# Performance work log

Measured on AMD Instinct MI355X. Metric: run time of the kernel, lower is better.

## Reference

```python
import jax, jax.numpy as jnp
import numpy as np
import math

N_HEADS = 16
D_Q = 1024
D_K = 1024
D_V = 1024
D_OUT = 1024
HID = D_OUT // N_HEADS  # 64
BATCH = 2
SEQ = 2048


def setup_inputs() -> dict:
    key = jax.random.key(0)
    ks = jax.random.split(key, 7)
    stdv = 1.0 / math.sqrt(HID)
    so = 1.0 / math.sqrt(D_OUT)
    return {
        "q": jax.random.normal(ks[0], (BATCH, SEQ, D_Q), dtype=jnp.float32),
        "k": jax.random.normal(ks[1], (BATCH, SEQ, D_K), dtype=jnp.float32),
        "v": jax.random.normal(ks[2], (BATCH, SEQ, D_V), dtype=jnp.float32),
        "W_query": jax.random.uniform(ks[3], (N_HEADS, D_Q, HID), jnp.float32, -stdv, stdv),
        "W_key": jax.random.uniform(ks[4], (N_HEADS, D_K, HID), jnp.float32, -stdv, stdv),
        "W_val": jax.random.uniform(ks[5], (N_HEADS, D_V, HID), jnp.float32, -stdv, stdv),
        "W_out": jax.random.uniform(ks[6], (N_HEADS, HID, D_OUT), jnp.float32, -so, so),
    }


def reference(q, k, v, W_query, W_key, W_val, W_out):
    norm = 1.0 / math.sqrt(HID)
    # per-head projections: [h, b, s, e]
    Q = jnp.einsum("bqd,hde->hbqe", q, W_query)
    K = jnp.einsum("bkd,hde->hbke", k, W_key)
    V = jnp.einsum("bkd,hde->hbke", v, W_val)
    # scaled dot-product attention
    compat = norm * jnp.einsum("hbqe,hbke->hbqk", Q, K)
    attn = jax.nn.softmax(compat, axis=-1)
    heads = jnp.einsum("hbqk,hbke->hbqe", attn, V)
    # output projection: concat heads then W_out == sum over h of per-head proj
    out = jnp.einsum("hbqe,heo->bqo", heads, W_out)
    return out
```

## Files before the change

### kernel.cpp

```cpp
#include <hip/hip_runtime.h>
#include <hip/hip_bf16.h>

typedef __bf16 bf16;
typedef __bf16 bf16x8 __attribute__((ext_vector_type(8)));
typedef __bf16 bf16x4 __attribute__((ext_vector_type(4)));
typedef float  f32x4  __attribute__((ext_vector_type(4)));

#define MFMA16(a,b,c) __builtin_amdgcn_mfma_f32_16x16x32_bf16(a, b, c, 0, 0, 0)

__device__ __forceinline__ void gl2lds16(const bf16* g, bf16* l) {
    __builtin_amdgcn_global_load_lds(
        (__attribute__((address_space(1))) void*)g,
        (__attribute__((address_space(3))) void*)l, 16, 0, 0);
}

__global__ __launch_bounds__(256)
void prep_kernel(const float* __restrict__ q, const float* __restrict__ k,
                 const float* __restrict__ v, const float* __restrict__ Wq,
                 const float* __restrict__ Wk, const float* __restrict__ Wv,
                 const float* __restrict__ Wo, bf16* __restrict__ Xcat,
                 bf16* __restrict__ Wqkv, bf16* __restrict__ Wot)
{
    __shared__ bf16 Tl[64][72];
    const int bid = blockIdx.x;
    const int tid = threadIdx.x;

    if (bid < 6144) {
        int gidx = bid * 256 + tid;
        int t    = gidx >> 19;
        int off  = (gidx & 0x7FFFF) * 8;
        const float* src = (t == 0) ? q : (t == 1) ? k : v;
        const float4 f0 = *(const float4*)&src[off];
        const float4 f1 = *(const float4*)&src[off + 4];
        bf16x8 p = { (bf16)f0.x, (bf16)f0.y, (bf16)f0.z, (bf16)f0.w,
                     (bf16)f1.x, (bf16)f1.y, (bf16)f1.z, (bf16)f1.w };
        *(bf16x8*)&Xcat[(size_t)gidx * 8] = p;
        return;
    }
    if (bid < 6912) {
        int idx = bid - 6144;
        int x = idx & 15, z = idx >> 4;
        int t = z >> 4, h = z & 15;
        const float* inp = ((t == 0) ? Wq : (t == 1) ? Wk : Wv) + (size_t)h * 65536;
        bf16* outp = Wqkv + (size_t)t * 1024 * 1024 + (size_t)h * 65536;
        int r0 = x * 64;
        #pragma unroll
        for (int i = 0; i < 2; i++) {
            int s = tid + i * 256;
            int r = s >> 3, c8 = (s & 7) * 8;
            const float* ap = &inp[(size_t)(r0 + r) * 64 + c8];
            float4 f0 = *(const float4*)ap;
            float4 f1 = *(const float4*)(ap + 4);
            bf16x8 p = { (bf16)f0.x, (bf16)f0.y, (bf16)f0.z, (bf16)f0.w,
                         (bf16)f1.x, (bf16)f1.y, (bf16)f1.z, (bf16)f1.w };
            *(bf16x8*)&Tl[r][c8] = p;
        }
        __syncthreads();
        #pragma unroll
        for (int i = 0; i < 2; i++) {
            int s = tid + i * 256;
            int c = s >> 3, r8 = (s & 7) * 8;
            bf16x8 p;
            #pragma unroll
            for (int j = 0; j < 8; j++) p[j] = Tl[r8 + j][c];
            *(bf16x8*)&outp[(size_t)c * 1024 + r0 + r8] = p;
        }
        return;
    }
    {
        int idx = bid - 6912;
        int y = idx & 15, h = idx >> 4;
        int c0 = y * 64;
        const float* inp = Wo + (size_t)h * 65536;
        bf16* outp = Wot + (size_t)h * 64;
        #pragma unroll
        for (int i = 0; i < 2; i++) {
            int s = tid + i * 256;
            int r = s >> 3, c8 = (s & 7) * 8;
            const float* ap = &inp[(size_t)r * 1024 + c0 + c8];
            float4 f0 = *(const float4*)ap;
            float4 f1 = *(const float4*)(ap + 4);
            bf16x8 p = { (bf16)f0.x, (bf16)f0.y, (bf16)f0.z, (bf16)f0.w,
                         (bf16)f1.x, (bf16)f1.y, (bf16)f1.z, (bf16)f1.w };
            *(bf16x8*)&Tl[r][c8] = p;
        }
        __syncthreads();
        #pragma unroll
        for (int i = 0; i < 2; i++) {
            int s = tid + i * 256;
            int c = s >> 3, r8 = (s & 7) * 8;
            bf16x8 p;
            #pragma unroll
            for (int j = 0; j < 8; j++) p[j] = Tl[r8 + j][c];
            *(bf16x8*)&outp[(size_t)(c0 + c) * 1024 + r8] = p;
        }
    }
}

__global__ __launch_bounds__(256)
void qkv_gemm(const bf16* __restrict__ Xcat, const bf16* __restrict__ Wqkv,
              bf16* __restrict__ Cq, bf16* __restrict__ Ck, bf16* __restrict__ Vt,
              float qscale)
{
    __shared__ bf16 Al[128 * 64];
    __shared__ bf16 Bl[128 * 64];
    const int slab  = blockIdx.x >> 5;
    const int mbase = (blockIdx.x & 31) * 128;
    const int nbase = blockIdx.y * 128;
    const int tid = threadIdx.x;
    const int w = tid >> 6, lane = tid & 63;
    const int lm = lane & 15, q4 = lane >> 4;
    const int wr = (w >> 1) * 64, wc = (w & 1) * 64;
    const int lrow = lane >> 3, lsw = ((lane & 7) ^ lrow) * 8;

    const bf16* A  = Xcat + (size_t)slab * 4096 * 1024;
    const bf16* Bt = Wqkv + (size_t)slab * 1024 * 1024;

    f32x4 acc[4][4] = {};

    for (int k0 = 0; k0 < 1024; k0 += 64) {
        __syncthreads();
        #pragma unroll
        for (int i = 0; i < 4; i++) {
            int c = w * 4 + i;
            gl2lds16(&A [(size_t)(mbase + c * 8 + lrow) * 1024 + k0 + lsw], &Al[c * 512]);
            gl2lds16(&Bt[(size_t)(nbase + c * 8 + lrow) * 1024 + k0 + lsw], &Bl[c * 512]);
        }
        __syncthreads();
        #pragma unroll
        for (int kk2 = 0; kk2 < 2; kk2++) {
            bf16x8 a[4], bfr[4];
            const int g = ((kk2 * 4 + q4) ^ (lm & 7)) * 8;
            #pragma unroll
            for (int i = 0; i < 4; i++) a[i]   = *(const bf16x8*)&Al[(wr + i * 16 + lm) * 64 + g];
            #pragma unroll
            for (int j = 0; j < 4; j++) bfr[j] = *(const bf16x8*)&Bl[(wc + j * 16 + lm) * 64 + g];
            #pragma unroll
            for (int i = 0; i < 4; i++)
                #pragma unroll
                for (int j = 0; j < 4; j++)
                    acc[i][j] = MFMA16(a[i], bfr[j], acc[i][j]);
        }
    }

    if (slab == 2) {
        #pragma unroll
        for (int i = 0; i < 4; i++)
            #pragma unroll
            for (int j = 0; j < 4; j++) {
                int s0  = mbase + wr + i * 16 + q4 * 4;
                int col = nbase + wc + j * 16 + lm;
                int sp  = (s0 & ~31) | (((s0 >> 2) & 3) * 8) | (((s0 >> 4) & 1) * 4);
                bf16x4 p = { (bf16)acc[i][j][0], (bf16)acc[i][j][1],
                             (bf16)acc[i][j][2], (bf16)acc[i][j][3] };
                *(bf16x4*)&Vt[(size_t)col * 4096 + sp] = p;
            }
    } else {
        bf16* C = (slab == 0) ? Cq : Ck;
        const float scale = (slab == 0) ? qscale : 1.0f;
        #pragma unroll
        for (int i = 0; i < 4; i++)
            #pragma unroll
            for (int j = 0; j < 4; j++)
                #pragma unroll
                for (int r = 0; r < 4; r++) {
                    int row = mbase + wr + i * 16 + q4 * 4 + r;
                    int col = nbase + wc + j * 16 + lm;
                    C[(size_t)row * 1024 + col] = (bf16)(acc[i][j][r] * scale);
                }
    }
}

__global__ __launch_bounds__(256)
void outproj_gemm(const bf16* __restrict__ A, const bf16* __restrict__ Bt,
                  float* __restrict__ C)
{
    __shared__ bf16 Al[64 * 64];
    __shared__ bf16 Bl[128 * 64];
    const int mbase = blockIdx.x * 64;
    const int nbase = blockIdx.y * 128;
    const int tid = threadIdx.x;
    const int w = tid >> 6, lane = tid & 63;
    const int lm = lane & 15, q4 = lane >> 4;
    const int wm = (w >> 1) * 32, wn = (w & 1) * 64;
    const int lrow = lane >> 3, lsw = ((lane & 7) ^ lrow) * 8;

    f32x4 acc[2][4] = {};

    for (int k0 = 0; k0 < 1024; k0 += 64) {
        __syncthreads();
        #pragma unroll
        for (int i = 0; i < 2; i++) {
            int c = w * 2 + i;
            gl2lds16(&A[(size_t)(mbase + c * 8 + lrow) * 1024 + k0 + lsw], &Al[c * 512]);
        }
        #pragma unroll
        for (int i = 0; i < 4; i++) {
            int c = w * 4 + i;
            gl2lds16(&Bt[(size_t)(nbase + c * 8 + lrow) * 1024 + k0 + lsw], &Bl[c * 512]);
        }
        __syncthreads();
        #pragma unroll
        for (int kk2 = 0; kk2 < 2; kk2++) {
            bf16x8 a[2], bfr[4];
            const int g = ((kk2 * 4 + q4) ^ (lm & 7)) * 8;
            #pragma unroll
            for (int i = 0; i < 2; i++) a[i]   = *(const bf16x8*)&Al[(wm + i * 16 + lm) * 64 + g];
            #pragma unroll
            for (int j = 0; j < 4; j++) bfr[j] = *(const bf16x8*)&Bl[(wn + j * 16 + lm) * 64 + g];
            #pragma unroll
            for (int i = 0; i < 2; i++)
                #pragma unroll
                for (int j = 0; j < 4; j++)
                    acc[i][j] = MFMA16(a[i], bfr[j], acc[i][j]);
        }
    }

    #pragma unroll
    for (int i = 0; i < 2; i++)
        #pragma unroll
        for (int j = 0; j < 4; j++)
            #pragma unroll
            for (int r = 0; r < 4; r++) {
                int row = mbase + wm + i * 16 + q4 * 4 + r;
                int col = nbase + wn + j * 16 + lm;
                C[(size_t)row * 1024 + col] = acc[i][j][r];
            }
}

__global__ __launch_bounds__(256, 4)
void attn_kernel(const bf16* __restrict__ Qp, const bf16* __restrict__ Kp,
                 const bf16* __restrict__ Vt, bf16* __restrict__ Hd)
{
    __shared__ bf16 Kl[2][64 * 64];
    __shared__ bf16 Vl[2][64 * 64];

    const int n  = blockIdx.x + 32 * (blockIdx.y + 2 * blockIdx.z);
    const int m  = (n & 7) * 128 + (n >> 3);
    const int qt = m & 31, bh = m >> 5;
    const int b  = bh & 1,  h  = bh >> 1;

    const int qbase = qt * 64;
    const int tid  = threadIdx.x;
    const int w    = tid >> 6, lane = tid & 63;
    const int p    = w & 1;
    const int kvh  = w >> 1;
    const int lm   = lane & 15, q4 = lane >> 4;
    const int lrow = lane >> 3, lsw = ((lane & 7) ^ lrow) * 8;

    const bf16* Qh = Qp + (size_t)(b * 2048 + qbase + p * 32) * 1024 + h * 64;
    const bf16* Kh = Kp + (size_t)(b * 2048) * 1024 + h * 64;
    const bf16* Vh = Vt + (size_t)(h * 64) * 4096 + b * 2048;

    bf16x8 Qf[2][2];
    #pragma unroll
    for (int i = 0; i < 2; i++)
        #pragma unroll
        for (int kk2 = 0; kk2 < 2; kk2++)
            Qf[i][kk2] = *(const bf16x8*)&Qh[(size_t)(i * 16 + lm) * 1024 + kk2 * 32 + q4 * 8];

    const bf16 one = (bf16)1.0f;
    const bf16x8 ones = { one, one, one, one, one, one, one, one };

    f32x4 O[2][4] = {};
    f32x4 Lacc[2] = {};

    auto stage = [&](int kt, int d) {
        #pragma unroll
        for (int i = 0; i < 2; i++) {
            int c = w * 2 + i;
            gl2lds16(&Kh[(size_t)(kt * 64 + c * 8 + lrow) * 1024 + lsw], &Kl[d][c * 512]);
            gl2lds16(&Vh[(size_t)(c * 8 + lrow) * 4096 + kt * 64 + lsw], &Vl[d][c * 512]);
        }
    };

    stage(0, 0);

    for (int it = 0; it < 32; it++) {
        __syncthreads();
        if (it < 31) stage(it + 1, (it + 1) & 1);
        const bf16* Kd = &Kl[it & 1][0];
        const bf16* Vd = &Vl[it & 1][0];

        f32x4 St[2][2] = {};
        __builtin_amdgcn_s_setprio(1);
        #pragma unroll
        for (int c2 = 0; c2 < 2; c2++) {
            const int ctp = kvh * 2 + c2;
            #pragma unroll
            for (int kk2 = 0; kk2 < 2; kk2++) {
                const int g = ((kk2 * 4 + q4) ^ (lm & 7)) * 8;
                bf16x8 kf = *(const bf16x8*)&Kd[(ctp * 16 + lm) * 64 + g];
                #pragma unroll
                for (int i = 0; i < 2; i++)
                    St[i][c2] = MFMA16(kf, Qf[i][kk2], St[i][c2]);
            }
        }
        __builtin_amdgcn_s_setprio(0);

        bf16x8 Pf[2];
        #pragma unroll
        for (int i = 0; i < 2; i++)
            #pragma unroll
            for (int j = 0; j < 8; j++)
                Pf[i][j] = (bf16)__builtin_amdgcn_exp2f(St[i][j >> 2][j & 3]);

        __builtin_amdgcn_s_setprio(1);
        #pragma unroll
        for (int i = 0; i < 2; i++) Lacc[i] = MFMA16(Pf[i], ones, Lacc[i]);
        const int gv = ((kvh * 4 + q4) ^ (lm & 7)) * 8;
        #pragma unroll
        for (int et = 0; et < 4; et++) {
            bf16x8 vf = *(const bf16x8*)&Vd[(et * 16 + lm) * 64 + gv];
            #pragma unroll
            for (int i = 0; i < 2; i++)
                O[i][et] = MFMA16(Pf[i], vf, O[i][et]);
        }
        __builtin_amdgcn_s_setprio(0);
    }

    __syncthreads();
    float* Ol = (float*)&Kl[0][0];
    float* Ll = (float*)&Vl[0][0];
    if (kvh == 1) {
        #pragma unroll
        for (int i = 0; i < 2; i++)
            #pragma unroll
            for (int et = 0; et < 4; et++)
                #pragma unroll
                for (int r = 0; r < 4; r++)
                    Ol[p * 2048 + (i * 16 + q4 * 4 + r) * 64 + et * 16 + lm] = O[i][et][r];
        if (lm == 0) {
            #pragma unroll
            for (int i = 0; i < 2; i++)
                #pragma unroll
                for (int r = 0; r < 4; r++)
                    Ll[p * 32 + i * 16 + q4 * 4 + r] = Lacc[i][r];
        }
    }
    __syncthreads();
    if (kvh == 0) {
        #pragma unroll
        for (int i = 0; i < 2; i++) {
            float rl[4];
            #pragma unroll
            for (int r = 0; r < 4; r++)
                rl[r] = 1.0f / (Lacc[i][r] + Ll[p * 32 + i * 16 + q4 * 4 + r]);
            #pragma unroll
            for (int et = 0; et < 4; et++)
                #pragma unroll
                for (int r = 0; r < 4; r++) {
                    float o = O[i][et][r] +
                              Ol[p * 2048 + (i * 16 + q4 * 4 + r) * 64 + et * 16 + lm];
                    int row = b * 2048 + qbase + p * 32 + i * 16 + q4 * 4 + r;
                    Hd[(size_t)row * 1024 + h * 64 + et * 16 + lm] = (bf16)(o * rl[r]);
                }
        }
    }
}

extern "C" void kernel_launch(void* const* d_in, const int* in_sizes, int n_in,
                              void* d_out, int out_size, void* d_ws, size_t ws_size,
                              hipStream_t stream)
{
    const float* q  = (const float*)d_in[0];
    const float* k  = (const float*)d_in[1];
    const float* v  = (const float*)d_in[2];
    const float* Wq = (const float*)d_in[3];
    const float* Wk = (const float*)d_in[4];
    const float* Wv = (const float*)d_in[5];
    const float* Wo = (const float*)d_in[6];
    float* out = (float*)d_out;

    const size_t Mi = 1024 * 1024;
    bf16* Xcat  = (bf16*)d_ws;
    bf16* Hd    = Xcat;
    bf16* Wqkv  = Xcat + 12 * Mi;
    bf16* Wot   = Xcat + 15 * Mi;
    bf16* Qproj = Xcat + 16 * Mi;
    bf16* Kproj = Xcat + 20 * Mi;
    bf16* Vtb   = (bf16*)d_out;

    const float qscale = 0.125f * 1.4426950408889634f;

    prep_kernel<<<7168, 256, 0, stream>>>(q, k, v, Wq, Wk, Wv, Wo, Xcat, Wqkv, Wot);
    qkv_gemm<<<dim3(96, 8), 256, 0, stream>>>(Xcat, Wqkv, Qproj, Kproj, Vtb, qscale);
    attn_kernel<<<dim3(32, 2, 16), 256, 0, stream>>>(Qproj, Kproj, Vtb, Hd);
    outproj_gemm<<<dim3(64, 8), 256, 0, stream>>>(Hd, Wot, out);
}
```

Before: 211.0 us.

## Double-buffer LDS tiles in QKV and output-projection GEMMs

Both projection GEMMs now keep two LDS buffers per operand. The global-to-LDS load for the next k-tile is issued right after the barrier, so it overlaps with the MFMA work on the current tile, and there is one barrier per iteration instead of two. Wave priority is raised around the MFMA section. The cost is double the shared memory: 64KB per block in the QKV GEMM, which may lower occupancy.

```diff
diff --git a/kernel.cpp b/kernel.cpp
--- a/kernel.cpp
+++ b/kernel.cpp
@@ -102,8 +102,8 @@
               bf16* __restrict__ Cq, bf16* __restrict__ Ck, bf16* __restrict__ Vt,
               float qscale)
 {
-    __shared__ bf16 Al[128 * 64];
-    __shared__ bf16 Bl[128 * 64];
+    __shared__ bf16 Al[2][128 * 64];
+    __shared__ bf16 Bl[2][128 * 64];
     const int slab  = blockIdx.x >> 5;
     const int mbase = (blockIdx.x & 31) * 128;
     const int nbase = blockIdx.y * 128;
@@ -118,29 +118,38 @@
 
     f32x4 acc[4][4] = {};
 
-    for (int k0 = 0; k0 < 1024; k0 += 64) {
-        __syncthreads();
+    auto stage = [&](int k0, int d) {
         #pragma unroll
         for (int i = 0; i < 4; i++) {
             int c = w * 4 + i;
-            gl2lds16(&A [(size_t)(mbase + c * 8 + lrow) * 1024 + k0 + lsw], &Al[c * 512]);
-            gl2lds16(&Bt[(size_t)(nbase + c * 8 + lrow) * 1024 + k0 + lsw], &Bl[c * 512]);
-        }
+            gl2lds16(&A [(size_t)(mbase + c * 8 + lrow) * 1024 + k0 + lsw], &Al[d][c * 512]);
+            gl2lds16(&Bt[(size_t)(nbase + c * 8 + lrow) * 1024 + k0 + lsw], &Bl[d][c * 512]);
+        }
+    };
+
+    stage(0, 0);
+
+    for (int t = 0; t < 16; t++) {
         __syncthreads();
+        if (t < 15) stage((t + 1) * 64, (t + 1) & 1);
+        const bf16* Ad = &Al[t & 1][0];
+        const bf16* Bd = &Bl[t & 1][0];
+        __builtin_amdgcn_s_setprio(1);
         #pragma unroll
         for (int kk2 = 0; kk2 < 2; kk2++) {
             bf16x8 a[4], bfr[4];
             const int g = ((kk2 * 4 + q4) ^ (lm & 7)) * 8;
             #pragma unroll
-            for (int i = 0; i < 4; i++) a[i]   = *(const bf16x8*)&Al[(wr + i * 16 + lm) * 64 + g];
-            #pragma unroll
-            for (int j = 0; j < 4; j++) bfr[j] = *(const bf16x8*)&Bl[(wc + j * 16 + lm) * 64 + g];
+            for (int i = 0; i < 4; i++) a[i]   = *(const bf16x8*)&Ad[(wr + i * 16 + lm) * 64 + g];
+            #pragma unroll
+            for (int j = 0; j < 4; j++) bfr[j] = *(const bf16x8*)&Bd[(wc + j * 16 + lm) * 64 + g];
             #pragma unroll
             for (int i = 0; i < 4; i++)
                 #pragma unroll
                 for (int j = 0; j < 4; j++)
                     acc[i][j] = MFMA16(a[i], bfr[j], acc[i][j]);
         }
+        __builtin_amdgcn_s_setprio(0);
     }
 
     if (slab == 2) {
@@ -175,8 +184,8 @@
 void outproj_gemm(const bf16* __restrict__ A, const bf16* __restrict__ Bt,
                   float* __restrict__ C)
 {
-    __shared__ bf16 Al[64 * 64];
-    __shared__ bf16 Bl[128 * 64];
+    __shared__ bf16 Al[2][64 * 64];
+    __shared__ bf16 Bl[2][128 * 64];
     const int mbase = blockIdx.x * 64;
     const int nbase = blockIdx.y * 128;
     const int tid = threadIdx.x;
@@ -187,33 +196,42 @@
 
     f32x4 acc[2][4] = {};
 
-    for (int k0 = 0; k0 < 1024; k0 += 64) {
-        __syncthreads();
+    auto stage = [&](int k0, int d) {
         #pragma unroll
         for (int i = 0; i < 2; i++) {
             int c = w * 2 + i;
-            gl2lds16(&A[(size_t)(mbase + c * 8 + lrow) * 1024 + k0 + lsw], &Al[c * 512]);
+            gl2lds16(&A[(size_t)(mbase + c * 8 + lrow) * 1024 + k0 + lsw], &Al[d][c * 512]);
         }
         #pragma unroll
         for (int i = 0; i < 4; i++) {
             int c = w * 4 + i;
-            gl2lds16(&Bt[(size_t)(nbase + c * 8 + lrow) * 1024 + k0 + lsw], &Bl[c * 512]);
-        }
+            gl2lds16(&Bt[(size_t)(nbase + c * 8 + lrow) * 1024 + k0 + lsw], &Bl[d][c * 512]);
+        }
+    };
+
+    stage(0, 0);
+
+    for (int t = 0; t < 16; t++) {
         __syncthreads();
+        if (t < 15) stage((t + 1) * 64, (t + 1) & 1);
+        const bf16* Ad = &Al[t & 1][0];
+        const bf16* Bd = &Bl[t & 1][0];
+        __builtin_amdgcn_s_setprio(1);
         #pragma unroll
         for (int kk2 = 0; kk2 < 2; kk2++) {
             bf16x8 a[2], bfr[4];
             const int g = ((kk2 * 4 + q4) ^ (lm & 7)) * 8;
             #pragma unroll
-            for (int i = 0; i < 2; i++) a[i]   = *(const bf16x8*)&Al[(wm + i * 16 + lm) * 64 + g];
-            #pragma unroll
-            for (int j = 0; j < 4; j++) bfr[j] = *(const bf16x8*)&Bl[(wn + j * 16 + lm) * 64 + g];
+            for (int i = 0; i < 2; i++) a[i]   = *(const bf16x8*)&Ad[(wm + i * 16 + lm) * 64 + g];
+            #pragma unroll
+            for (int j = 0; j < 4; j++) bfr[j] = *(const bf16x8*)&Bd[(wn + j * 16 + lm) * 64 + g];
             #pragma unroll
             for (int i = 0; i < 2; i++)
                 #pragma unroll
                 for (int j = 0; j < 4; j++)
                     acc[i][j] = MFMA16(a[i], bfr[j], acc[i][j]);
         }
+        __builtin_amdgcn_s_setprio(0);
     }
 
     #pragma unroll
```

Result: faster. 203.9 us (-3.3%).
